# Kernel optimization log

Measured on AMD Instinct MI355X. Metric: run time of the kernel, lower is better.

Reference implementation:

```python
import jax, jax.numpy as jnp
import numpy as np

B, LQ, LKV = 32, 512, 512
SIZE, H = 512, 8
HD = SIZE // H
SCALE = 1.0 / np.sqrt(HD)
LN_EPS = 1e-5


def layer_norm(x, w, b):
    mu = jnp.mean(x, axis=-1, keepdims=True)
    var = jnp.mean(jnp.square(x - mu), axis=-1, keepdims=True)
    return (x - mu) * jax.lax.rsqrt(var + LN_EPS) * w + b


def setup_inputs() -> dict:
    key = jax.random.key(0)
    ks = jax.random.split(key, 8)
    s = 0.02
    return {
        "query": jax.random.normal(ks[0], (B, LQ, SIZE), jnp.float32),
        "key_value": jax.random.normal(ks[1], (B, LKV, SIZE), jnp.float32),
        "Wq": jax.random.normal(ks[2], (SIZE, SIZE), jnp.float32) * s,
        "bq": jnp.zeros((SIZE,), jnp.float32),
        "Wk": jax.random.normal(ks[3], (SIZE, SIZE), jnp.float32) * s,
        "bk": jnp.zeros((SIZE,), jnp.float32),
        "Wv": jax.random.normal(ks[4], (SIZE, SIZE), jnp.float32) * s,
        "bv": jnp.zeros((SIZE,), jnp.float32),
        "Wo": jax.random.normal(ks[5], (SIZE, SIZE), jnp.float32) * s,
        "bo": jnp.zeros((SIZE,), jnp.float32),
        "ln0_w": jnp.ones((SIZE,), jnp.float32),
        "ln0_b": jnp.zeros((SIZE,), jnp.float32),
        "ln1_w": jnp.ones((SIZE,), jnp.float32),
        "ln1_b": jnp.zeros((SIZE,), jnp.float32),
    }


def reference(query, key_value, Wq, bq, Wk, bk, Wv, bv, Wo, bo, ln0_w, ln0_b, ln1_w, ln1_b):
    b, lq, _ = query.shape
    lkv = key_value.shape[1]
    # projections
    q = query @ Wq.T + bq          # [B, Lq, SIZE]
    k = key_value @ Wk.T + bk      # [B, Lkv, SIZE]
    v = key_value @ Wv.T + bv
    # split heads: torch cat(split(head_size, 2), 0) == [B,L,H,HD] view with head axis separate
    qh = q.reshape(b, lq, H, HD)
    kh = k.reshape(b, lkv, H, HD)
    vh = v.reshape(b, lkv, H, HD)
    # attention scores [B, H, Lq, Lkv]
    A_ = jnp.einsum("bqhd,bkhd->bhqk", qh, kh) * SCALE
    # signed softmax: tanh(A_) * softmax(sqrt(A_^2 + 0.01)) over keys
    A = jnp.tanh(A_) * jax.nn.softmax(jnp.sqrt(jnp.square(A_) + 0.01), axis=-1)
    # residual q + attention output, merge heads back
    oh = qh + jnp.einsum("bhqk,bkhd->bqhd", A, vh)   # [B, Lq, H, HD]
    output = oh.reshape(b, lq, SIZE)
    output = layer_norm(output, ln0_w, ln0_b)
    output = output + jax.nn.relu(output @ Wo.T + bo)
    output = layer_norm(output, ln1_w, ln1_b)
    return output
```

## Files before the change

kernel.cpp:

```cpp
#include <hip/hip_runtime.h>

#define SIZE_D 512
#define HEADS  8
#define HDIM   64
#define BATCH  32
#define SEQ    512
#define SCALE_F 0.125f
#define NROWS  (BATCH * SEQ)

typedef __attribute__((ext_vector_type(8))) short bf16x8;
typedef __attribute__((ext_vector_type(4))) float f32x4;
typedef __attribute__((ext_vector_type(4))) unsigned int u32x4;

__device__ __forceinline__ unsigned short f2bf(float f) {
    union { float f; unsigned int u; } c{f};
    unsigned int x = c.u;
    x += 0x7fffu + ((x >> 16) & 1u);
    return (unsigned short)(x >> 16);
}
__device__ __forceinline__ float bf2f(unsigned short u) {
    union { unsigned int i; float f; } c;
    c.i = (unsigned int)u << 16;
    return c.f;
}
__device__ __forceinline__ unsigned int pack2bf(float lo, float hi) {
    return ((__float_as_uint(hi) + 0x8000u) & 0xffff0000u) |
           ((__float_as_uint(lo) + 0x8000u) >> 16);
}
__device__ __forceinline__ void gload_lds16(const unsigned short* g, unsigned short* l) {
    __builtin_amdgcn_global_load_lds(
        (const __attribute__((address_space(1))) unsigned int*)g,
        (__attribute__((address_space(3))) unsigned int*)l, 16, 0, 0);
}

#define KBAR8() do {                                                      \
    asm volatile("s_waitcnt vmcnt(8) lgkmcnt(0)" ::: "memory");           \
    __builtin_amdgcn_sched_barrier(0);                                    \
    __builtin_amdgcn_s_barrier();                                         \
    __builtin_amdgcn_sched_barrier(0);                                    \
} while (0)
#define KBAR0() do {                                                      \
    asm volatile("s_waitcnt vmcnt(0) lgkmcnt(0)" ::: "memory");           \
    __builtin_amdgcn_sched_barrier(0);                                    \
    __builtin_amdgcn_s_barrier();                                         \
    __builtin_amdgcn_sched_barrier(0);                                    \
} while (0)

__global__ __launch_bounds__(256) void cvt_w4(const float* __restrict__ w0,
                                              const float* __restrict__ w1,
                                              const float* __restrict__ w2,
                                              const float* __restrict__ w3,
                                              unsigned short* __restrict__ d) {
    const float* srcs[4] = {w0, w1, w2, w3};
    const float* s = srcs[blockIdx.y];
    unsigned short* dst = d + (size_t)blockIdx.y * (SIZE_D * SIZE_D);
    const int n = SIZE_D * SIZE_D;
    const int stride = gridDim.x * blockDim.x * 4;
    for (int i = (blockIdx.x * blockDim.x + threadIdx.x) * 4; i < n; i += stride) {
        const float4 v = *reinterpret_cast<const float4*>(s + i);
        ushort4 o;
        o.x = f2bf(v.x); o.y = f2bf(v.y); o.z = f2bf(v.z); o.w = f2bf(v.w);
        *reinterpret_cast<ushort4*>(dst + i) = o;
    }
}

__global__ __launch_bounds__(256, 2) void gemm_proj3(const float* __restrict__ query,
                                                     const float* __restrict__ keyv,
                                                     const unsigned short* __restrict__ Wall,
                                                     const float* __restrict__ bq,
                                                     const float* __restrict__ bk,
                                                     const float* __restrict__ bv,
                                                     unsigned short* __restrict__ Qh,
                                                     unsigned short* __restrict__ Kh,
                                                     unsigned short* __restrict__ Vt) {
    __shared__ __align__(16) unsigned short Ad[2][128 * 64];
    __shared__ __align__(16) unsigned short Bd[2][128 * 64];

    const int tid  = threadIdx.x;
    const int wv   = tid >> 6;
    const int lane = tid & 63;
    const int y    = blockIdx.y;
    const int bm   = blockIdx.x * 128;
    const int bn   = y * 128;
    const int wr   = wv >> 1;
    const int wc   = wv & 1;

    const float* A = (y < 4) ? query : keyv;

    float4 areg[2][4][2];

    auto loadA = [&](int t, int slot) {
        const int k0 = t * 64;
#pragma unroll
        for (int i = 0; i < 4; ++i) {
            const int o   = (wv * 32 + i * 8) * 128 + lane * 16;
            const int row = o >> 7;
            const int col = ((o & 127) ^ ((row & 7) << 4)) >> 1;
            const float* src = A + (size_t)(bm + row) * SIZE_D + k0 + col;
            areg[slot][i][0] = *reinterpret_cast<const float4*>(src);
            areg[slot][i][1] = *reinterpret_cast<const float4*>(src + 4);
        }
    };
    auto writeA = [&](int buf, int slot) {
#pragma unroll
        for (int i = 0; i < 4; ++i) {
            const int o = (wv * 32 + i * 8) * 128 + lane * 16;
            union { unsigned int u[4]; bf16x8 v; } pk;
            pk.u[0] = pack2bf(areg[slot][i][0].x, areg[slot][i][0].y);
            pk.u[1] = pack2bf(areg[slot][i][0].z, areg[slot][i][0].w);
            pk.u[2] = pack2bf(areg[slot][i][1].x, areg[slot][i][1].y);
            pk.u[3] = pack2bf(areg[slot][i][1].z, areg[slot][i][1].w);
            *reinterpret_cast<bf16x8*>(&Ad[buf][o >> 1]) = pk.v;
        }
    };
    auto stageW = [&](int buf, int t) {
        const int k0 = t * 64;
#pragma unroll
        for (int i = 0; i < 4; ++i) {
            const int o   = (wv * 32 + i * 8) * 128 + lane * 16;
            const int row = o >> 7;
            const int col = ((o & 127) ^ ((row & 7) << 4)) >> 1;
            gload_lds16(Wall + (size_t)(bn + row) * SIZE_D + k0 + col, &Bd[buf][o >> 1]);
        }
    };

    f32x4 acc[4][4];
#pragma unroll
    for (int mt = 0; mt < 4; ++mt)
#pragma unroll
        for (int nt = 0; nt < 4; ++nt) acc[mt][nt] = (f32x4){0.f, 0.f, 0.f, 0.f};

    loadA(0, 0);
    stageW(0, 0);
    writeA(0, 0);
    loadA(1, 1);

#pragma unroll
    for (int t = 0; t < 8; ++t) {
        const int cur = t & 1;
        if (t < 7) { KBAR8(); } else { KBAR0(); }

        if (t < 7) stageW(cur ^ 1, t + 1);
        if (t < 6) loadA(t + 2, t & 1);

        bf16x8 af[2][4], bfr[2][4];
#pragma unroll
        for (int kc = 0; kc < 2; ++kc) {
#pragma unroll
            for (int mt = 0; mt < 4; ++mt) {
                const int r = wr * 64 + mt * 16 + (lane & 15);
                int byte = r * 128 + kc * 64 + (lane >> 4) * 16;
                byte ^= (r & 7) << 4;
                af[kc][mt] = *reinterpret_cast<const bf16x8*>(
                    reinterpret_cast<const char*>(&Ad[cur][0]) + byte);
            }
#pragma unroll
            for (int nt = 0; nt < 4; ++nt) {
                const int r = wc * 64 + nt * 16 + (lane & 15);
                int byte = r * 128 + kc * 64 + (lane >> 4) * 16;
                byte ^= (r & 7) << 4;
                bfr[kc][nt] = *reinterpret_cast<const bf16x8*>(
                    reinterpret_cast<const char*>(&Bd[cur][0]) + byte);
            }
        }
#pragma unroll
        for (int kc = 0; kc < 2; ++kc)
#pragma unroll
            for (int mt = 0; mt < 4; ++mt)
#pragma unroll
                for (int nt = 0; nt < 4; ++nt)
                    acc[mt][nt] = __builtin_amdgcn_mfma_f32_16x16x32_bf16(
                        af[kc][mt], bfr[kc][nt], acc[mt][nt], 0, 0, 0);

        if (t < 7) writeA(cur ^ 1, (t + 1) & 1);
    }

    if (y < 8) {
        const float* bias = (y < 4) ? bq : bk;
        unsigned short* D = (y < 4) ? Qh : Kh;
        const int coff = (y < 4) ? 0 : 512;
#pragma unroll
        for (int nt = 0; nt < 4; ++nt) {
            const int colL = bn - coff + wc * 64 + nt * 16 + (lane & 15);
            const float bc = bias[colL];
            const int h = colL >> 6, dd = colL & 63;
#pragma unroll
            for (int mt = 0; mt < 4; ++mt) {
                const int row0 = bm + wr * 64 + mt * 16 + (lane >> 4) * 4;
#pragma unroll
                for (int r = 0; r < 4; ++r) {
                    const int row = row0 + r;
                    const int b_ = row >> 9, l = row & 511;
                    float z = acc[mt][nt][r] + bc;
                    if (y >= 4) z *= SCALE_F;
                    D[(((size_t)b_ * HEADS + h) * SEQ + l) * HDIM + dd] = f2bf(z);
                }
            }
        }
    } else {
#pragma unroll
        for (int nt = 0; nt < 4; ++nt) {
            const int c2 = bn - 1024 + wc * 64 + nt * 16 + (lane & 15);
            const float bc = bv[c2];
            const int hV = c2 >> 6, dV = c2 & 63;
#pragma unroll
            for (int mt = 0; mt < 4; ++mt) {
                const int row0 = bm + wr * 64 + mt * 16 + (lane >> 4) * 4;
                const int b_ = row0 >> 9, kv = row0 & 511;
                ushort4 pk;
                pk.x = f2bf(acc[mt][nt][0] + bc);
                pk.y = f2bf(acc[mt][nt][1] + bc);
                pk.z = f2bf(acc[mt][nt][2] + bc);
                pk.w = f2bf(acc[mt][nt][3] + bc);
                *reinterpret_cast<ushort4*>(
                    &Vt[(((size_t)b_ * HEADS + hV) * HDIM + dV) * SEQ + kv]) = pk;
            }
        }
    }
}

__global__ __launch_bounds__(256, 2) void attn_mfma(const unsigned short* __restrict__ Qh,
                                                    const unsigned short* __restrict__ Kh,
                                                    const unsigned short* __restrict__ Vt,
                                                    unsigned short* __restrict__ outb) {
    __shared__ __align__(16) unsigned short Kt[4][64 * 64];
    __shared__ __align__(16) unsigned short Vs[4][64 * 64];

    const int tid  = threadIdx.x;
    const int wv   = tid >> 6;
    const int lane = tid & 63;
    const int bh   = blockIdx.x;
    const int b    = bh >> 3;
    const int h    = bh & 7;
    const int g    = lane >> 4;

    const unsigned short* Qb = Qh + (size_t)bh * (SEQ * HDIM);
    const unsigned short* Kb = Kh + (size_t)bh * (SEQ * HDIM);
    const unsigned short* Vb = Vt + (size_t)bh * (HDIM * SEQ);

    const int m0 = blockIdx.y * 256 + wv * 64;

    auto stageKV = [&](int buf, int t) {
        const int kv0 = t * 64;
#pragma unroll
        for (int i = 0; i < 2; ++i) {
            const int o   = i * 4096 + tid * 16;
            const int row = o >> 7;
            const int in  = (o & 127) ^ ((row & 7) << 4);
            gload_lds16(Kb + (size_t)(kv0 + row) * HDIM + (in >> 1), &Kt[buf][o >> 1]);
            gload_lds16(Vb + (size_t)row * SEQ + kv0 + (in >> 1), &Vs[buf][o >> 1]);
        }
    };

    bf16x8 qf[4][2];
#pragma unroll
    for (int mt = 0; mt < 4; ++mt)
#pragma unroll
        for (int kc = 0; kc < 2; ++kc) {
            const int m = m0 + mt * 16 + (lane & 15);
            union { u32x4 u; bf16x8 v; } cv;
            cv.u = *reinterpret_cast<const u32x4*>(
                Qb + (size_t)m * HDIM + kc * 32 + g * 8);
            qf[mt][kc] = cv.v;
        }

    f32x4 oacc[4][4];
    float esum[4] = {0.f, 0.f, 0.f, 0.f};
#pragma unroll
    for (int mt = 0; mt < 4; ++mt)
#pragma unroll
        for (int x = 0; x < 4; ++x) oacc[mt][x] = (f32x4){0.f, 0.f, 0.f, 0.f};

    stageKV(0, 0);
    stageKV(1, 1);
    __syncthreads();

    for (int tt = 0; tt < 8; tt += 2) {
        if (tt < 6) {
            stageKV((tt + 2) & 3, tt + 2);
            stageKV((tt + 3) & 3, tt + 3);
        }

#pragma unroll
        for (int p = 0; p < 2; ++p) {
            const int cur = (tt + p) & 3;

            f32x4 sacc[4][4];
#pragma unroll
            for (int nt = 0; nt < 4; ++nt)
#pragma unroll
                for (int mt = 0; mt < 4; ++mt) sacc[nt][mt] = (f32x4){0.f, 0.f, 0.f, 0.f};

#pragma unroll
            for (int kc = 0; kc < 2; ++kc) {
                bf16x8 kf[4];
#pragma unroll
                for (int nt = 0; nt < 4; ++nt) {
                    const int kvl = nt * 16 + (lane & 15);
                    int byte = kvl * 128 + kc * 64 + g * 16;
                    byte ^= (kvl & 7) << 4;
                    kf[nt] = *reinterpret_cast<const bf16x8*>(
                        reinterpret_cast<const char*>(&Kt[cur][0]) + byte);
                }
                __builtin_amdgcn_s_setprio(1);
#pragma unroll
                for (int nt = 0; nt < 4; ++nt)
#pragma unroll
                    for (int mt = 0; mt < 4; ++mt)
                        sacc[nt][mt] = __builtin_amdgcn_mfma_f32_16x16x32_bf16(
                            kf[nt], qf[mt][kc], sacc[nt][mt], 0, 0, 0);
                __builtin_amdgcn_s_setprio(0);
            }

            bf16x8 pa[2][4];
#pragma unroll
            for (int c = 0; c < 2; ++c)
#pragma unroll
                for (int mt = 0; mt < 4; ++mt) {
                    float w[8];
#pragma unroll
                    for (int j = 0; j < 8; ++j) {
                        const float s  = sacc[2 * c + (j >> 2)][mt][j & 3];
                        const float a  = fabsf(s);
                        const float tt_ = __expf(a);
                        const float t2 = tt_ * tt_;
                        const float u  = __builtin_amdgcn_sqrtf(fmaf(s, s, 0.01f));
                        const float dl = u - a;
                        const float ed = fmaf(dl, fmaf(dl, 0.5f, 1.0f), 1.0f);
                        const float eu = tt_ * ed;
                        esum[mt] += eu;
                        const float th = fmaf(-2.0f, __builtin_amdgcn_rcpf(t2 + 1.0f), 1.0f);
                        w[j] = __builtin_copysignf(th * eu, s);
                    }
                    union { unsigned int u[4]; bf16x8 v; } pk;
#pragma unroll
                    for (int pp = 0; pp < 4; ++pp)
                        pk.u[pp] = (__float_as_uint(w[2 * pp + 1]) & 0xffff0000u) |
                                   (__float_as_uint(w[2 * pp]) >> 16);
                    pa[c][mt] = pk.v;
                }

#pragma unroll
            for (int c = 0; c < 2; ++c) {
                bf16x8 vf[4];
#pragma unroll
                for (int dt = 0; dt < 4; ++dt) {
                    const int d = dt * 16 + (lane & 15);
                    const int swz = (d & 7) << 4;
                    const int rowb = d * 128;
                    uint2 lo = *reinterpret_cast<const uint2*>(
                        reinterpret_cast<const char*>(&Vs[cur][0]) +
                        (rowb + (((c * 32 + 4 * g) * 2) ^ swz)));
                    uint2 hi = *reinterpret_cast<const uint2*>(
                        reinterpret_cast<const char*>(&Vs[cur][0]) +
                        (rowb + (((c * 32 + 16 + 4 * g) * 2) ^ swz)));
                    union { unsigned int u[4]; bf16x8 v; } cvb;
                    cvb.u[0] = lo.x; cvb.u[1] = lo.y;
                    cvb.u[2] = hi.x; cvb.u[3] = hi.y;
                    vf[dt] = cvb.v;
                }
                __builtin_amdgcn_s_setprio(1);
#pragma unroll
                for (int mt = 0; mt < 4; ++mt)
#pragma unroll
                    for (int dt = 0; dt < 4; ++dt)
                        oacc[mt][dt] = __builtin_amdgcn_mfma_f32_16x16x32_bf16(
                            pa[c][mt], vf[dt], oacc[mt][dt], 0, 0, 0);
                __builtin_amdgcn_s_setprio(0);
            }
        }

        __syncthreads();
    }

    float rden[4];
#pragma unroll
    for (int mt = 0; mt < 4; ++mt) {
        float e = esum[mt];
        e += __shfl_xor(e, 16);
        e += __shfl_xor(e, 32);
        rden[mt] = __builtin_amdgcn_rcpf(e);
    }
    float rr_[4][4];
#pragma unroll
    for (int mt = 0; mt < 4; ++mt)
#pragma unroll
        for (int r = 0; r < 4; ++r)
            rr_[mt][r] = __shfl(rden[mt], g * 4 + r);

#pragma unroll
    for (int mt = 0; mt < 4; ++mt)
#pragma unroll
        for (int dt = 0; dt < 4; ++dt)
#pragma unroll
            for (int r = 0; r < 4; ++r) {
                const int m = m0 + mt * 16 + g * 4 + r;
                const int d = dt * 16 + (lane & 15);
                const float qv = bf2f(Qb[(size_t)m * HDIM + d]);
                outb[((size_t)b * SEQ + m) * SIZE_D + h * HDIM + d] =
                    f2bf(qv + oacc[mt][dt][r] * rr_[mt][r]);
            }
}

__global__ __launch_bounds__(256) void ln0_bf16(const unsigned short* __restrict__ in,
                                                const float* __restrict__ w,
                                                const float* __restrict__ b,
                                                unsigned short* __restrict__ outb) {
    const int tid  = threadIdx.x;
    const int lane = tid & 63;
    const int row  = blockIdx.x * 4 + (tid >> 6);
    const size_t base = (size_t)row * SIZE_D + lane * 8;

    const ushort4 a0 = *reinterpret_cast<const ushort4*>(&in[base]);
    const ushort4 a1 = *reinterpret_cast<const ushort4*>(&in[base + 4]);
    float x[8];
    x[0] = bf2f(a0.x); x[1] = bf2f(a0.y); x[2] = bf2f(a0.z); x[3] = bf2f(a0.w);
    x[4] = bf2f(a1.x); x[5] = bf2f(a1.y); x[6] = bf2f(a1.z); x[7] = bf2f(a1.w);

    float s = 0.f, sq = 0.f;
#pragma unroll
    for (int j = 0; j < 8; ++j) { s += x[j]; sq += x[j] * x[j]; }
#pragma unroll
    for (int off = 32; off > 0; off >>= 1) {
        s  += __shfl_xor(s, off);
        sq += __shfl_xor(sq, off);
    }

    const float mu  = s * (1.0f / SIZE_D);
    const float var = sq * (1.0f / SIZE_D) - mu * mu;
    const float rr  = rsqrtf(var + 1e-5f);

    const float4 w0 = *reinterpret_cast<const float4*>(&w[lane * 8]);
    const float4 w1 = *reinterpret_cast<const float4*>(&w[lane * 8 + 4]);
    const float4 b0 = *reinterpret_cast<const float4*>(&b[lane * 8]);
    const float4 b1 = *reinterpret_cast<const float4*>(&b[lane * 8 + 4]);
    const float wa[8] = {w0.x, w0.y, w0.z, w0.w, w1.x, w1.y, w1.z, w1.w};
    const float ba[8] = {b0.x, b0.y, b0.z, b0.w, b1.x, b1.y, b1.z, b1.w};

    union { unsigned short s[8]; bf16x8 v; } o;
#pragma unroll
    for (int j = 0; j < 8; ++j)
        o.s[j] = f2bf((x[j] - mu) * rr * wa[j] + ba[j]);
    *reinterpret_cast<bf16x8*>(&outb[base]) = o.v;
}

__global__ __launch_bounds__(512, 2) void oproj_ln(const unsigned short* __restrict__ X,
                                                   const unsigned short* __restrict__ W,
                                                   const float* __restrict__ bo,
                                                   const float* __restrict__ g1,
                                                   const float* __restrict__ b1,
                                                   float* __restrict__ out) {
    __shared__ __align__(16) unsigned short Ad[2][32 * 32];
    __shared__ __align__(16) unsigned short Bd[2][512 * 32];
    __shared__ float red[32][8][2];
    __shared__ float stat[32][2];

    const int tid  = threadIdx.x;
    const int wv   = tid >> 6;
    const int lane = tid & 63;
    const int bm   = blockIdx.x * 32;

    auto stage = [&](int buf, int t) {
        const int k0 = t * 32;
        if (tid < 128) {
            const int o   = tid * 16;
            const int row = o >> 6;
            const int in  = (o & 63) ^ (((row >> 1) & 3) << 4);
            gload_lds16(X + (size_t)(bm + row) * SIZE_D + k0 + (in >> 1), &Ad[buf][o >> 1]);
        }
#pragma unroll
        for (int i = 0; i < 4; ++i) {
            const int o   = i * 8192 + tid * 16;
            const int row = o >> 6;
            const int in  = (o & 63) ^ (((row >> 1) & 3) << 4);
            gload_lds16(W + (size_t)row * SIZE_D + k0 + (in >> 1), &Bd[buf][o >> 1]);
        }
    };

    f32x4 acc[2][4];
#pragma unroll
    for (int mt = 0; mt < 2; ++mt)
#pragma unroll
        for (int nt = 0; nt < 4; ++nt) acc[mt][nt] = (f32x4){0.f, 0.f, 0.f, 0.f};

    stage(0, 0);
    __syncthreads();
    int cur = 0;

    for (int t = 0; t < 16; ++t) {
        if (t < 15) stage(cur ^ 1, t + 1);

        bf16x8 af[2], bfr[4];
#pragma unroll
        for (int mt = 0; mt < 2; ++mt) {
            const int r = mt * 16 + (lane & 15);
            int byte = r * 64 + (lane >> 4) * 16;
            byte ^= ((r >> 1) & 3) << 4;
            af[mt] = *reinterpret_cast<const bf16x8*>(
                reinterpret_cast<const char*>(&Ad[cur][0]) + byte);
        }
#pragma unroll
        for (int nt = 0; nt < 4; ++nt) {
            const int r = wv * 64 + nt * 16 + (lane & 15);
            int byte = r * 64 + (lane >> 4) * 16;
            byte ^= ((r >> 1) & 3) << 4;
            bfr[nt] = *reinterpret_cast<const bf16x8*>(
                reinterpret_cast<const char*>(&Bd[cur][0]) + byte);
        }
#pragma unroll
        for (int mt = 0; mt < 2; ++mt)
#pragma unroll
            for (int nt = 0; nt < 4; ++nt)
                acc[mt][nt] = __builtin_amdgcn_mfma_f32_16x16x32_bf16(
                    af[mt], bfr[nt], acc[mt][nt], 0, 0, 0);

        __syncthreads();
        cur ^= 1;
    }

#pragma unroll
    for (int nt = 0; nt < 4; ++nt) {
        const int n  = wv * 64 + nt * 16 + (lane & 15);
        const float bc = bo[n];
#pragma unroll
        for (int mt = 0; mt < 2; ++mt) {
            const int row0 = bm + mt * 16 + (lane >> 4) * 4;
#pragma unroll
            for (int r = 0; r < 4; ++r) {
                const float R = bf2f(X[(size_t)(row0 + r) * SIZE_D + n]);
                acc[mt][nt][r] = R + fmaxf(acc[mt][nt][r] + bc, 0.0f);
            }
        }
    }

    float ps[2][4], pq[2][4];
#pragma unroll
    for (int mt = 0; mt < 2; ++mt)
#pragma unroll
        for (int r = 0; r < 4; ++r) {
            float s = 0.f, q = 0.f;
#pragma unroll
            for (int nt = 0; nt < 4; ++nt) {
                const float v = acc[mt][nt][r];
                s += v; q += v * v;
            }
#pragma unroll
            for (int off = 1; off <= 8; off <<= 1) {
                s += __shfl_xor(s, off);
                q += __shfl_xor(q, off);
            }
            ps[mt][r] = s; pq[mt][r] = q;
        }
    if ((lane & 15) < 8) {
        const int mtw = (lane & 15) >> 2;
        const int rw  = lane & 3;
        const int rowL = mtw * 16 + (lane >> 4) * 4 + rw;
        red[rowL][wv][0] = ps[mtw][rw];
        red[rowL][wv][1] = pq[mtw][rw];
    }
    __syncthreads();
    if (tid < 32) {
        float s = 0.f, q = 0.f;
#pragma unroll
        for (int w8 = 0; w8 < 8; ++w8) { s += red[tid][w8][0]; q += red[tid][w8][1]; }
        const float mu  = s * (1.0f / SIZE_D);
        const float var = q * (1.0f / SIZE_D) - mu * mu;
        stat[tid][0] = mu;
        stat[tid][1] = rsqrtf(var + 1e-5f);
    }
    __syncthreads();

#pragma unroll
    for (int nt = 0; nt < 4; ++nt) {
        const int n = wv * 64 + nt * 16 + (lane & 15);
        const float g = g1[n], bb = b1[n];
#pragma unroll
        for (int mt = 0; mt < 2; ++mt) {
#pragma unroll
            for (int r = 0; r < 4; ++r) {
                const int rowL = mt * 16 + (lane >> 4) * 4 + r;
                const float y = (acc[mt][nt][r] - stat[rowL][0]) * stat[rowL][1];
                out[(size_t)(bm + rowL) * SIZE_D + n] = y * g + bb;
            }
        }
    }
}

extern "C" void kernel_launch(void* const* d_in, const int* in_sizes, int n_in,
                              void* d_out, int out_size, void* d_ws, size_t ws_size,
                              hipStream_t stream) {
    const float* query = (const float*)d_in[0];
    const float* keyv  = (const float*)d_in[1];
    const float* Wq    = (const float*)d_in[2];
    const float* bq    = (const float*)d_in[3];
    const float* Wk    = (const float*)d_in[4];
    const float* bk    = (const float*)d_in[5];
    const float* Wv    = (const float*)d_in[6];
    const float* bv    = (const float*)d_in[7];
    const float* Wo    = (const float*)d_in[8];
    const float* bo    = (const float*)d_in[9];
    const float* ln0w  = (const float*)d_in[10];
    const float* ln0b  = (const float*)d_in[11];
    const float* ln1w  = (const float*)d_in[12];
    const float* ln1b  = (const float*)d_in[13];
    float* out = (float*)d_out;

    char* ws = (char*)d_ws;
    unsigned short* obf  = (unsigned short*)ws;
    unsigned short* Qh   = (unsigned short*)(ws + ((size_t)32 << 20));
    unsigned short* Xbf  = Qh;
    unsigned short* Kh   = (unsigned short*)(ws + ((size_t)48 << 20));
    unsigned short* Vt   = (unsigned short*)(ws + ((size_t)64 << 20));
    unsigned short* Wbf  = (unsigned short*)(ws + ((size_t)80 << 20));
    unsigned short* WoB  = Wbf + 786432;

    cvt_w4<<<dim3(64, 4), 256, 0, stream>>>(Wq, Wk, Wv, Wo, Wbf);

    gemm_proj3<<<dim3(128, 12), 256, 0, stream>>>(query, keyv, Wbf, bq, bk, bv, Qh, Kh, Vt);

    attn_mfma<<<dim3(BATCH * HEADS, 2), 256, 0, stream>>>(Qh, Kh, Vt, obf);

    ln0_bf16<<<NROWS / 4, 256, 0, stream>>>(obf, ln0w, ln0b, Xbf);

    oproj_ln<<<NROWS / 32, 512, 0, stream>>>(Xbf, WoB, bo, ln1w, ln1b, out);
}
```

Before: 146.9 us.

## Restructure projection GEMM into a 4-stage, BK=32 pipeline with paired k-steps

The QKV projection GEMM moves from double-buffered 64-wide K tiles to four 32-wide LDS stages. Each iteration of the main loop now handles two k-steps, so the loop has half as many block barriers, and a plain __syncthreads replaces the hand-tuned waitcnt barrier macros. The LDS swizzle is rewritten for 64-byte rows. The goal is fewer barriers and more global-load latency hidden behind MFMA work. In exchange, the coarser __syncthreads drains all outstanding loads at the end of each iteration, which may cut into the intended overlap.

```diff
diff --git a/kernel.cpp b/kernel.cpp
--- a/kernel.cpp
+++ b/kernel.cpp
@@ -32,19 +32,6 @@
         (const __attribute__((address_space(1))) unsigned int*)g,
         (__attribute__((address_space(3))) unsigned int*)l, 16, 0, 0);
 }
-
-#define KBAR8() do {                                                      \
-    asm volatile("s_waitcnt vmcnt(8) lgkmcnt(0)" ::: "memory");           \
-    __builtin_amdgcn_sched_barrier(0);                                    \
-    __builtin_amdgcn_s_barrier();                                         \
-    __builtin_amdgcn_sched_barrier(0);                                    \
-} while (0)
-#define KBAR0() do {                                                      \
-    asm volatile("s_waitcnt vmcnt(0) lgkmcnt(0)" ::: "memory");           \
-    __builtin_amdgcn_sched_barrier(0);                                    \
-    __builtin_amdgcn_s_barrier();                                         \
-    __builtin_amdgcn_sched_barrier(0);                                    \
-} while (0)
 
 __global__ __launch_bounds__(256) void cvt_w4(const float* __restrict__ w0,
                                               const float* __restrict__ w1,
@@ -73,12 +60,13 @@
                                                      unsigned short* __restrict__ Qh,
                                                      unsigned short* __restrict__ Kh,
                                                      unsigned short* __restrict__ Vt) {
-    __shared__ __align__(16) unsigned short Ad[2][128 * 64];
-    __shared__ __align__(16) unsigned short Bd[2][128 * 64];
+    __shared__ __align__(16) unsigned short Ad[4][128 * 32];
+    __shared__ __align__(16) unsigned short Bd[4][128 * 32];
 
     const int tid  = threadIdx.x;
     const int wv   = tid >> 6;
     const int lane = tid & 63;
+    const int g    = lane >> 4;
     const int y    = blockIdx.y;
     const int bm   = blockIdx.x * 128;
     const int bn   = y * 128;
@@ -87,15 +75,15 @@
 
     const float* A = (y < 4) ? query : keyv;
 
-    float4 areg[2][4][2];
+    float4 areg[2][2][2];
 
     auto loadA = [&](int t, int slot) {
-        const int k0 = t * 64;
-#pragma unroll
-        for (int i = 0; i < 4; ++i) {
-            const int o   = (wv * 32 + i * 8) * 128 + lane * 16;
-            const int row = o >> 7;
-            const int col = ((o & 127) ^ ((row & 7) << 4)) >> 1;
+        const int k0 = t * 32;
+#pragma unroll
+        for (int i = 0; i < 2; ++i) {
+            const int o   = i * 4096 + tid * 16;
+            const int row = o >> 6;
+            const int col = ((o & 63) ^ (((row >> 1) & 3) << 4)) >> 1;
             const float* src = A + (size_t)(bm + row) * SIZE_D + k0 + col;
             areg[slot][i][0] = *reinterpret_cast<const float4*>(src);
             areg[slot][i][1] = *reinterpret_cast<const float4*>(src + 4);
@@ -103,8 +91,8 @@
     };
     auto writeA = [&](int buf, int slot) {
 #pragma unroll
-        for (int i = 0; i < 4; ++i) {
-            const int o = (wv * 32 + i * 8) * 128 + lane * 16;
+        for (int i = 0; i < 2; ++i) {
+            const int o = i * 4096 + tid * 16;
             union { unsigned int u[4]; bf16x8 v; } pk;
             pk.u[0] = pack2bf(areg[slot][i][0].x, areg[slot][i][0].y);
             pk.u[1] = pack2bf(areg[slot][i][0].z, areg[slot][i][0].w);
@@ -114,12 +102,12 @@
         }
     };
     auto stageW = [&](int buf, int t) {
-        const int k0 = t * 64;
-#pragma unroll
-        for (int i = 0; i < 4; ++i) {
-            const int o   = (wv * 32 + i * 8) * 128 + lane * 16;
-            const int row = o >> 7;
-            const int col = ((o & 127) ^ ((row & 7) << 4)) >> 1;
+        const int k0 = t * 32;
+#pragma unroll
+        for (int i = 0; i < 2; ++i) {
+            const int o   = i * 4096 + tid * 16;
+            const int row = o >> 6;
+            const int col = ((o & 63) ^ (((row >> 1) & 3) << 4)) >> 1;
             gload_lds16(Wall + (size_t)(bn + row) * SIZE_D + k0 + col, &Bd[buf][o >> 1]);
         }
     };
@@ -130,49 +118,54 @@
 #pragma unroll
         for (int nt = 0; nt < 4; ++nt) acc[mt][nt] = (f32x4){0.f, 0.f, 0.f, 0.f};
 
+    auto compute = [&](int buf) {
+        bf16x8 af[4], bfr[4];
+#pragma unroll
+        for (int mt = 0; mt < 4; ++mt) {
+            const int r = wr * 64 + mt * 16 + (lane & 15);
+            int byte = r * 64 + g * 16;
+            byte ^= ((r >> 1) & 3) << 4;
+            af[mt] = *reinterpret_cast<const bf16x8*>(
+                reinterpret_cast<const char*>(&Ad[buf][0]) + byte);
+        }
+#pragma unroll
+        for (int nt = 0; nt < 4; ++nt) {
+            const int r = wc * 64 + nt * 16 + (lane & 15);
+            int byte = r * 64 + g * 16;
+            byte ^= ((r >> 1) & 3) << 4;
+            bfr[nt] = *reinterpret_cast<const bf16x8*>(
+                reinterpret_cast<const char*>(&Bd[buf][0]) + byte);
+        }
+#pragma unroll
+        for (int mt = 0; mt < 4; ++mt)
+#pragma unroll
+            for (int nt = 0; nt < 4; ++nt)
+                acc[mt][nt] = __builtin_amdgcn_mfma_f32_16x16x32_bf16(
+                    af[mt], bfr[nt], acc[mt][nt], 0, 0, 0);
+    };
+
     loadA(0, 0);
+    loadA(1, 1);
     stageW(0, 0);
+    stageW(1, 1);
     writeA(0, 0);
-    loadA(1, 1);
-
-#pragma unroll
-    for (int t = 0; t < 8; ++t) {
-        const int cur = t & 1;
-        if (t < 7) { KBAR8(); } else { KBAR0(); }
-
-        if (t < 7) stageW(cur ^ 1, t + 1);
-        if (t < 6) loadA(t + 2, t & 1);
-
-        bf16x8 af[2][4], bfr[2][4];
-#pragma unroll
-        for (int kc = 0; kc < 2; ++kc) {
-#pragma unroll
-            for (int mt = 0; mt < 4; ++mt) {
-                const int r = wr * 64 + mt * 16 + (lane & 15);
-                int byte = r * 128 + kc * 64 + (lane >> 4) * 16;
-                byte ^= (r & 7) << 4;
-                af[kc][mt] = *reinterpret_cast<const bf16x8*>(
-                    reinterpret_cast<const char*>(&Ad[cur][0]) + byte);
-            }
-#pragma unroll
-            for (int nt = 0; nt < 4; ++nt) {
-                const int r = wc * 64 + nt * 16 + (lane & 15);
-                int byte = r * 128 + kc * 64 + (lane >> 4) * 16;
-                byte ^= (r & 7) << 4;
-                bfr[kc][nt] = *reinterpret_cast<const bf16x8*>(
-                    reinterpret_cast<const char*>(&Bd[cur][0]) + byte);
-            }
-        }
-#pragma unroll
-        for (int kc = 0; kc < 2; ++kc)
-#pragma unroll
-            for (int mt = 0; mt < 4; ++mt)
-#pragma unroll
-                for (int nt = 0; nt < 4; ++nt)
-                    acc[mt][nt] = __builtin_amdgcn_mfma_f32_16x16x32_bf16(
-                        af[kc][mt], bfr[kc][nt], acc[mt][nt], 0, 0, 0);
-
-        if (t < 7) writeA(cur ^ 1, (t + 1) & 1);
+    writeA(1, 1);
+    __syncthreads();
+
+    for (int tt = 0; tt < 16; tt += 2) {
+        if (tt < 14) {
+            loadA(tt + 2, 0);
+            loadA(tt + 3, 1);
+            stageW((tt + 2) & 3, tt + 2);
+            stageW((tt + 3) & 3, tt + 3);
+        }
+
+        compute(tt & 3);
+        if (tt < 14) writeA((tt + 2) & 3, 0);
+        compute((tt + 1) & 3);
+        if (tt < 14) writeA((tt + 3) & 3, 1);
+
+        __syncthreads();
     }
 
     if (y < 8) {
@@ -186,7 +179,7 @@
             const int h = colL >> 6, dd = colL & 63;
 #pragma unroll
             for (int mt = 0; mt < 4; ++mt) {
-                const int row0 = bm + wr * 64 + mt * 16 + (lane >> 4) * 4;
+                const int row0 = bm + wr * 64 + mt * 16 + g * 4;
 #pragma unroll
                 for (int r = 0; r < 4; ++r) {
                     const int row = row0 + r;
@@ -205,7 +198,7 @@
             const int hV = c2 >> 6, dV = c2 & 63;
 #pragma unroll
             for (int mt = 0; mt < 4; ++mt) {
-                const int row0 = bm + wr * 64 + mt * 16 + (lane >> 4) * 4;
+                const int row0 = bm + wr * 64 + mt * 16 + g * 4;
                 const int b_ = row0 >> 9, kv = row0 & 511;
                 ushort4 pk;
                 pk.x = f2bf(acc[mt][nt][0] + bc);
```

Result: slower. 151.9 us (+3.4%).
